# Kernel optimization log

Hardware: AMD Instinct MI355X
Metric: run time of the kernel (lower is better)

## Reference

```python
import jax, jax.numpy as jnp
import numpy as np

N = 50000       # nodes
E = 600000      # edges
F_IN = 500      # num_feature
H = 64          # hidden_dim (ODE state = 2*H)
C = 40          # num_class
T = 1.0         # integration time
STEPS = 4       # RK4 steps (16 ODE function evals)


def setup_inputs() -> dict:
    key = jax.random.key(0)
    ks = jax.random.split(key, 7)
    x = jax.random.normal(ks[0], (N, F_IN), dtype=jnp.float32)
    edge_src = jax.random.randint(ks[1], (E,), 0, N, dtype=jnp.int32)
    edge_dst = jax.random.randint(ks[2], (E,), 0, N, dtype=jnp.int32)
    edge_w = jax.random.uniform(ks[3], (E,), dtype=jnp.float32)
    m1_w = jax.random.normal(ks[4], (F_IN, H), dtype=jnp.float32) / np.sqrt(F_IN).astype(np.float32)
    m1_b = jnp.zeros((H,), jnp.float32)
    alpha_train = jnp.ones((N,), jnp.float32)  # alpha * ones(N) with alpha=1.0
    m2_w = jax.random.normal(ks[5], (H, C), dtype=jnp.float32) / np.sqrt(H).astype(np.float32)
    m2_b = jnp.zeros((C,), jnp.float32)
    return dict(x=x, edge_w=edge_w, m1_w=m1_w, m1_b=m1_b,
                alpha_train=alpha_train, m2_w=m2_w, m2_b=m2_b,
                edge_src=edge_src, edge_dst=edge_dst)


def spmm(edge_src, edge_dst, edge_w, z):
    # A @ z where A[i,j] = sum of edge_w over edges (src=i, dst=j)
    msg = edge_w[:, None] * z[edge_dst]           # [E, 2H]
    return jax.ops.segment_sum(msg, edge_src, num_segments=N)


def reference(x, edge_w, m1_w, m1_b, alpha_train, m2_w, m2_b, edge_src, edge_dst):
    # Encoder (dropout is identity in eval mode)
    h = x @ m1_w + m1_b                           # [N, H]
    h = jnp.concatenate([h, jnp.zeros_like(h)], axis=1)  # [N, 2H]
    x0 = jax.lax.stop_gradient(h)                 # x0 = x.clone().detach()
    alph = jax.nn.sigmoid(alpha_train)[:, None]   # [N, 1]

    def f(z):  # ODE RHS: sigmoid(alpha)*0.5*(A z - z) + x0
        az = spmm(edge_src, edge_dst, edge_w, z)
        return alph * 0.5 * (az - z) + x0

    dt = jnp.float32(T / STEPS)

    def step(z, _):
        k1 = f(z)
        k2 = f(z + 0.5 * dt * k1)
        k3 = f(z + 0.5 * dt * k2)
        k4 = f(z + dt * k3)
        return z + (dt / 6.0) * (k1 + 2.0 * k2 + 2.0 * k3 + k4), None

    z, _ = jax.lax.scan(step, h, None, length=STEPS)
    z = jax.nn.relu(z[:, :H])                     # first half of state
    return z @ m2_w + m2_b                        # [N, C]
```

## Files before the change

### kernel.cpp

```cpp
#include <hip/hip_runtime.h>
#include <hip/hip_fp16.h>

#define N_NODES 50000
#define N_EDGES 600000
#define F_IN    500
#define H_DIM   64
#define C_OUT   40
#define STEPS   4
#define NB_SCAN ((N_NODES + 255) / 256)
#define KTILES  16
#define DBINS   64

using half8 = __attribute__((ext_vector_type(8))) _Float16;
using f32x4 = __attribute__((ext_vector_type(4))) float;

__global__ __launch_bounds__(256) void bfrag_kernel(
    const float* __restrict__ W, __half* __restrict__ bfrag)
{
    int t = blockIdx.x * 256 + threadIdx.x;
    if (t >= KTILES * 4 * 64) return;
    int lane = t & 63;
    int c    = (t >> 6) & 3;
    int kt   = t >> 8;
    int col  = c * 16 + (lane & 15);
    int kb   = kt * 32 + (lane >> 4) * 8;
    union { uint4 u; __half h[8]; } v;
    #pragma unroll
    for (int j = 0; j < 8; ++j) {
        int k = kb + j;
        v.h[j] = (k < F_IN) ? __float2half(W[(size_t)k * H_DIM + col]) : __half(0.f);
    }
    *reinterpret_cast<uint4*>(bfrag + (size_t)t * 8) = v.u;
}

__global__ __launch_bounds__(256) void encoder_kernel(
    const float* __restrict__ x, const __half* __restrict__ bfrag,
    const float* __restrict__ b, __half* __restrict__ x0H,
    float* __restrict__ zF, __half* __restrict__ zH)
{
    __shared__ f32x4 red[2][64][4];

    int wave = threadIdx.x >> 6;
    int lane = threadIdx.x & 63;
    int pair = wave >> 1;
    int half = wave & 1;
    int rowl = lane & 15;
    int kg   = lane >> 4;
    int r0   = blockIdx.x * 32 + pair * 16;

    int gr = r0 + rowl; if (gr >= N_NODES) gr = N_NODES - 1;
    const float* xrow = x + (size_t)gr * F_IN;
    const uint4* bf = reinterpret_cast<const uint4*>(bfrag);

    int ktb = half * 8;

    float4 xv[16];
    #pragma unroll
    for (int ki = 0; ki < 8; ++ki) {
        int k0 = (ktb + ki) * 32 + kg * 8;
        xv[2 * ki]     = make_float4(0.f, 0.f, 0.f, 0.f);
        xv[2 * ki + 1] = make_float4(0.f, 0.f, 0.f, 0.f);
        if (k0 + 4 <= F_IN) xv[2 * ki]     = *reinterpret_cast<const float4*>(xrow + k0);
        if (k0 + 8 <= F_IN) xv[2 * ki + 1] = *reinterpret_cast<const float4*>(xrow + k0 + 4);
    }

    f32x4 acc[4];
    #pragma unroll
    for (int c = 0; c < 4; ++c) acc[c] = (f32x4){0.f, 0.f, 0.f, 0.f};

    #pragma unroll
    for (int ki = 0; ki < 8; ++ki) {
        int kt = ktb + ki;
        float4 xa = xv[2 * ki], xb = xv[2 * ki + 1];
        half8 a;
        a[0] = (_Float16)xa.x; a[1] = (_Float16)xa.y;
        a[2] = (_Float16)xa.z; a[3] = (_Float16)xa.w;
        a[4] = (_Float16)xb.x; a[5] = (_Float16)xb.y;
        a[6] = (_Float16)xb.z; a[7] = (_Float16)xb.w;
        #pragma unroll
        for (int c = 0; c < 4; ++c) {
            union { uint4 u; half8 h; } bv;
            bv.u = bf[(size_t)(kt * 4 + c) * 64 + lane];
            acc[c] = __builtin_amdgcn_mfma_f32_16x16x32_f16(a, bv.h, acc[c], 0, 0, 0);
        }
    }

    if (half == 1) {
        #pragma unroll
        for (int c = 0; c < 4; ++c) red[pair][lane][c] = acc[c];
    }
    __syncthreads();
    if (half == 0) {
        #pragma unroll
        for (int c = 0; c < 4; ++c) {
            f32x4 r = red[pair][lane][c];
            acc[c][0] += r[0]; acc[c][1] += r[1];
            acc[c][2] += r[2]; acc[c][3] += r[3];
        }
        #pragma unroll
        for (int c = 0; c < 4; ++c) {
            int col = c * 16 + rowl;
            float bias = b[col];
            #pragma unroll
            for (int r = 0; r < 4; ++r) {
                int grow = r0 + kg * 4 + r;
                if (grow < N_NODES) {
                    float v = acc[c][r] + bias;
                    size_t idx = (size_t)grow * H_DIM + col;
                    zF[idx]  = v;
                    __half hv = __float2half(v);
                    zH[idx]  = hv;
                    x0H[idx] = hv;
                }
            }
        }
    }
}

__global__ void hist_kernel(const int* __restrict__ src, int* __restrict__ counts)
{
    int e = blockIdx.x * 256 + threadIdx.x;
    if (e < N_EDGES) atomicAdd(&counts[src[e]], 1);
}

__global__ __launch_bounds__(256) void scanA_kernel(
    const int* __restrict__ counts, int* __restrict__ blockSums)
{
    __shared__ int red[256];
    int i = blockIdx.x * 256 + threadIdx.x;
    red[threadIdx.x] = (i < N_NODES) ? counts[i] : 0;
    __syncthreads();
    #pragma unroll
    for (int s = 128; s > 0; s >>= 1) {
        if (threadIdx.x < s) red[threadIdx.x] += red[threadIdx.x + s];
        __syncthreads();
    }
    if (threadIdx.x == 0) blockSums[blockIdx.x] = red[0];
}

__global__ __launch_bounds__(256) void scanB_kernel(
    const int* __restrict__ blockSums, int* __restrict__ blockBases)
{
    __shared__ int s[256];
    int tid = threadIdx.x;
    int v = (tid < NB_SCAN) ? blockSums[tid] : 0;
    s[tid] = v;
    __syncthreads();
    #pragma unroll
    for (int d = 1; d < 256; d <<= 1) {
        int t = (tid >= d) ? s[tid - d] : 0;
        __syncthreads();
        s[tid] += t;
        __syncthreads();
    }
    if (tid < NB_SCAN) blockBases[tid] = s[tid] - v;
}

__global__ __launch_bounds__(256) void scanC_kernel(
    const int* __restrict__ counts, const int* __restrict__ blockBases,
    int* __restrict__ off, int* __restrict__ cursor)
{
    __shared__ int s[256];
    int tid = threadIdx.x;
    int i = blockIdx.x * 256 + tid;
    int v = (i < N_NODES) ? counts[i] : 0;
    s[tid] = v;
    __syncthreads();
    #pragma unroll
    for (int d = 1; d < 256; d <<= 1) {
        int t = (tid >= d) ? s[tid - d] : 0;
        __syncthreads();
        s[tid] += t;
        __syncthreads();
    }
    if (i < N_NODES) {
        int excl = blockBases[blockIdx.x] + s[tid] - v;
        off[i] = excl;
        cursor[i] = excl;
        if (i == N_NODES - 1) off[N_NODES] = excl + v;
    }
}

__global__ void scatter_kernel(const int* __restrict__ src, const int* __restrict__ dst,
                               const float* __restrict__ w,
                               int* __restrict__ cursor, int2* __restrict__ epack)
{
    int e = blockIdx.x * 256 + threadIdx.x;
    if (e < N_EDGES) {
        int s = src[e];
        int p = atomicAdd(&cursor[s], 1);
        epack[p] = make_int2(dst[e] << 7, __float_as_int(w[e]));
    }
}

__global__ __launch_bounds__(256) void blockHist_kernel(
    const int* __restrict__ counts, int* __restrict__ blockBinCnt)
{
    __shared__ int lh[DBINS];
    int t = threadIdx.x;
    if (t < DBINS) lh[t] = 0;
    __syncthreads();
    int i = blockIdx.x * 256 + t;
    if (i < N_NODES) {
        int d = counts[i]; if (d > DBINS - 1) d = DBINS - 1;
        atomicAdd(&lh[d], 1);
    }
    __syncthreads();
    if (t < DBINS) blockBinCnt[blockIdx.x * DBINS + t] = lh[t];
}

__global__ __launch_bounds__(64) void degBase_kernel(
    const int* __restrict__ blockBinCnt, int* __restrict__ baseMat)
{
    __shared__ int tot[DBINS];
    __shared__ int start[DBINS];
    int d = threadIdx.x;
    int s = 0;
    for (int b = 0; b < NB_SCAN; ++b) s += blockBinCnt[b * DBINS + d];
    tot[d] = s;
    __syncthreads();
    if (d == 0) {
        int r = 0;
        for (int q = 0; q < DBINS; ++q) { start[q] = r; r += tot[q]; }
    }
    __syncthreads();
    int r = start[d];
    for (int b = 0; b < NB_SCAN; ++b) {
        baseMat[b * DBINS + d] = r;
        r += blockBinCnt[b * DBINS + d];
    }
}

__global__ __launch_bounds__(256) void degScatter_kernel(
    const int* __restrict__ counts, const int* __restrict__ baseMat,
    int* __restrict__ node_order)
{
    __shared__ int lcur[DBINS];
    int t = threadIdx.x;
    if (t < DBINS) lcur[t] = baseMat[blockIdx.x * DBINS + t];
    __syncthreads();
    int i = blockIdx.x * 256 + t;
    if (i < N_NODES) {
        int d = counts[i]; if (d > DBINS - 1) d = DBINS - 1;
        int p = atomicAdd(&lcur[d], 1);
        node_order[p] = i;
    }
}

template<int STAGE>
__global__ __launch_bounds__(256) void stage_kernel(
    const int* __restrict__ node_order,
    const int* __restrict__ off, const int2* __restrict__ epack,
    const __half* __restrict__ zsH, const __half* __restrict__ zH,
    const float* __restrict__ zbF, const __half* __restrict__ x0H,
    const float* __restrict__ alpha, __half* __restrict__ accH,
    __half* __restrict__ outH, float* __restrict__ outZ, float cnext)
{
    int nidx = blockIdx.x * 32 + (threadIdx.x >> 3);
    if (nidx >= N_NODES) return;
    int node = node_order[nidx];
    int cb = (threadIdx.x & 7) << 4;
    int c  = cb >> 1;

    int jb = off[node], je = off[node + 1];
    const char* rdB = reinterpret_cast<const char*>(zsH);

    union H4 { uint4 u; __half2 h[4]; };

    float azA[8], azB[8];
    #pragma unroll
    for (int i = 0; i < 8; ++i) { azA[i] = 0.f; azB[i] = 0.f; }

#define ACC8(dst, V, W)                                                    \
    {                                                                      \
        float2 f0 = __half22float2((V).h[0]);                              \
        float2 f1 = __half22float2((V).h[1]);                              \
        float2 f2 = __half22float2((V).h[2]);                              \
        float2 f3 = __half22float2((V).h[3]);                              \
        dst[0] = fmaf(W, f0.x, dst[0]); dst[1] = fmaf(W, f0.y, dst[1]);    \
        dst[2] = fmaf(W, f1.x, dst[2]); dst[3] = fmaf(W, f1.y, dst[3]);    \
        dst[4] = fmaf(W, f2.x, dst[4]); dst[5] = fmaf(W, f2.y, dst[5]);    \
        dst[6] = fmaf(W, f3.x, dst[6]); dst[7] = fmaf(W, f3.y, dst[7]);    \
    }

    int j = jb;
    for (; j + 3 < je; j += 4) {
        int2 e0 = epack[j];
        int2 e1 = epack[j + 1];
        int2 e2 = epack[j + 2];
        int2 e3 = epack[j + 3];
        H4 v0, v1, v2, v3;
        v0.u = *reinterpret_cast<const uint4*>(rdB + (size_t)(unsigned)e0.x + cb);
        v1.u = *reinterpret_cast<const uint4*>(rdB + (size_t)(unsigned)e1.x + cb);
        v2.u = *reinterpret_cast<const uint4*>(rdB + (size_t)(unsigned)e2.x + cb);
        v3.u = *reinterpret_cast<const uint4*>(rdB + (size_t)(unsigned)e3.x + cb);
        float w0 = __int_as_float(e0.y), w1 = __int_as_float(e1.y);
        float w2 = __int_as_float(e2.y), w3 = __int_as_float(e3.y);
        ACC8(azA, v0, w0);
        ACC8(azB, v1, w1);
        ACC8(azA, v2, w2);
        ACC8(azB, v3, w3);
    }
    for (; j < je; ++j) {
        int2 e0 = epack[j];
        H4 v0;
        v0.u = *reinterpret_cast<const uint4*>(rdB + (size_t)(unsigned)e0.x + cb);
        float w0 = __int_as_float(e0.y);
        ACC8(azA, v0, w0);
    }
#undef ACC8

    float az[8];
    #pragma unroll
    for (int i = 0; i < 8; ++i) az[i] = azA[i] + azB[i];

    size_t idx = (size_t)node * H_DIM + c;
    H4 sr; sr.u = *reinterpret_cast<const uint4*>(zsH + idx);
    float s[8];
    {
        float2 f0 = __half22float2(sr.h[0]), f1 = __half22float2(sr.h[1]);
        float2 f2 = __half22float2(sr.h[2]), f3 = __half22float2(sr.h[3]);
        s[0] = f0.x; s[1] = f0.y; s[2] = f1.x; s[3] = f1.y;
        s[4] = f2.x; s[5] = f2.y; s[6] = f3.x; s[7] = f3.y;
    }
    H4 xr; xr.u = *reinterpret_cast<const uint4*>(x0H + idx);
    float xv[8];
    {
        float2 f0 = __half22float2(xr.h[0]), f1 = __half22float2(xr.h[1]);
        float2 f2 = __half22float2(xr.h[2]), f3 = __half22float2(xr.h[3]);
        xv[0] = f0.x; xv[1] = f0.y; xv[2] = f1.x; xv[3] = f1.y;
        xv[4] = f2.x; xv[5] = f2.y; xv[6] = f3.x; xv[7] = f3.y;
    }
    float a = 0.5f / (1.f + __expf(-alpha[node]));

    float k[8];
    #pragma unroll
    for (int i = 0; i < 8; ++i) k[i] = fmaf(a, az[i] - s[i], xv[i]);

    float o[8];
    if constexpr (STAGE == 0) {
        H4 aw;
        aw.h[0] = __float22half2_rn(make_float2(k[0], k[1]));
        aw.h[1] = __float22half2_rn(make_float2(k[2], k[3]));
        aw.h[2] = __float22half2_rn(make_float2(k[4], k[5]));
        aw.h[3] = __float22half2_rn(make_float2(k[6], k[7]));
        *reinterpret_cast<uint4*>(accH + idx) = aw.u;
        #pragma unroll
        for (int i = 0; i < 8; ++i) o[i] = fmaf(cnext, k[i], s[i]);
    } else if constexpr (STAGE == 1 || STAGE == 2) {
        H4 ar; ar.u = *reinterpret_cast<const uint4*>(accH + idx);
        float av[8];
        {
            float2 f0 = __half22float2(ar.h[0]), f1 = __half22float2(ar.h[1]);
            float2 f2 = __half22float2(ar.h[2]), f3 = __half22float2(ar.h[3]);
            av[0] = f0.x; av[1] = f0.y; av[2] = f1.x; av[3] = f1.y;
            av[4] = f2.x; av[5] = f2.y; av[6] = f3.x; av[7] = f3.y;
        }
        #pragma unroll
        for (int i = 0; i < 8; ++i) av[i] = fmaf(2.f, k[i], av[i]);
        H4 aw;
        aw.h[0] = __float22half2_rn(make_float2(av[0], av[1]));
        aw.h[1] = __float22half2_rn(make_float2(av[2], av[3]));
        aw.h[2] = __float22half2_rn(make_float2(av[4], av[5]));
        aw.h[3] = __float22half2_rn(make_float2(av[6], av[7]));
        *reinterpret_cast<uint4*>(accH + idx) = aw.u;
        H4 br; br.u = *reinterpret_cast<const uint4*>(zH + idx);
        float bv[8];
        {
            float2 f0 = __half22float2(br.h[0]), f1 = __half22float2(br.h[1]);
            float2 f2 = __half22float2(br.h[2]), f3 = __half22float2(br.h[3]);
            bv[0] = f0.x; bv[1] = f0.y; bv[2] = f1.x; bv[3] = f1.y;
            bv[4] = f2.x; bv[5] = f2.y; bv[6] = f3.x; bv[7] = f3.y;
        }
        #pragma unroll
        for (int i = 0; i < 8; ++i) o[i] = fmaf(cnext, k[i], bv[i]);
    } else {
        H4 ar; ar.u = *reinterpret_cast<const uint4*>(accH + idx);
        float av[8];
        {
            float2 f0 = __half22float2(ar.h[0]), f1 = __half22float2(ar.h[1]);
            float2 f2 = __half22float2(ar.h[2]), f3 = __half22float2(ar.h[3]);
            av[0] = f0.x; av[1] = f0.y; av[2] = f1.x; av[3] = f1.y;
            av[4] = f2.x; av[5] = f2.y; av[6] = f3.x; av[7] = f3.y;
        }
        float4 zb0 = *reinterpret_cast<const float4*>(zbF + idx);
        float4 zb1 = *reinterpret_cast<const float4*>(zbF + idx + 4);
        float zb[8] = {zb0.x, zb0.y, zb0.z, zb0.w, zb1.x, zb1.y, zb1.z, zb1.w};
        #pragma unroll
        for (int i = 0; i < 8; ++i) o[i] = fmaf(cnext, av[i] + k[i], zb[i]);
        float4 oz0 = make_float4(o[0], o[1], o[2], o[3]);
        float4 oz1 = make_float4(o[4], o[5], o[6], o[7]);
        *reinterpret_cast<float4*>(outZ + idx)     = oz0;
        *reinterpret_cast<float4*>(outZ + idx + 4) = oz1;
    }
    H4 sv;
    sv.h[0] = __float22half2_rn(make_float2(o[0], o[1]));
    sv.h[1] = __float22half2_rn(make_float2(o[2], o[3]));
    sv.h[2] = __float22half2_rn(make_float2(o[4], o[5]));
    sv.h[3] = __float22half2_rn(make_float2(o[6], o[7]));
    *reinterpret_cast<uint4*>(outH + idx) = sv.u;
}

__global__ __launch_bounds__(256) void decoder_kernel(
    const float* __restrict__ z, const float* __restrict__ W2,
    const float* __restrict__ b2, float* __restrict__ out)
{
    __shared__ float zsm[4][H_DIM];
    int lane = threadIdx.x & 63;
    int w    = threadIdx.x >> 6;
    int node = blockIdx.x * 4 + w;
    int ld   = node >= N_NODES ? N_NODES - 1 : node;
    float zv = z[(size_t)ld * H_DIM + lane];
    zsm[w][lane] = zv > 0.f ? zv : 0.f;
    __syncthreads();
    if (node < N_NODES && lane < C_OUT) {
        float acc = b2[lane];
        #pragma unroll
        for (int k = 0; k < H_DIM; ++k)
            acc = fmaf(zsm[w][k], W2[k * C_OUT + lane], acc);
        out[(size_t)node * C_OUT + lane] = acc;
    }
}

extern "C" void kernel_launch(void* const* d_in, const int* in_sizes, int n_in,
                              void* d_out, int out_size, void* d_ws, size_t ws_size,
                              hipStream_t stream)
{
    const float* x     = (const float*)d_in[0];
    const float* ew    = (const float*)d_in[1];
    const float* m1w   = (const float*)d_in[2];
    const float* m1b   = (const float*)d_in[3];
    const float* alpha = (const float*)d_in[4];
    const float* m2w   = (const float*)d_in[5];
    const float* m2b   = (const float*)d_in[6];
    const int*   esrc  = (const int*)d_in[7];
    const int*   edst  = (const int*)d_in[8];
    float* out = (float*)d_out;

    char* ws = (char*)d_ws;
    size_t o = 0;
    auto alloc = [&](size_t bytes) -> void* {
        void* p = ws + o;
        o = (o + bytes + 255) & ~(size_t)255;
        return p;
    };
    float*  z      = (float*)alloc((size_t)N_NODES * H_DIM * 4);
    __half* x0H    = (__half*)alloc((size_t)N_NODES * H_DIM * 2);
    __half* zH     = (__half*)alloc((size_t)N_NODES * H_DIM * 2);
    __half* ztAH   = (__half*)alloc((size_t)N_NODES * H_DIM * 2);
    __half* ztBH   = (__half*)alloc((size_t)N_NODES * H_DIM * 2);
    __half* accH   = (__half*)alloc((size_t)N_NODES * H_DIM * 2);
    __half* bfrag  = (__half*)alloc((size_t)KTILES * 4 * 64 * 8 * 2);
    int*    counts = (int*)alloc((size_t)N_NODES * 4);
    int*    off    = (int*)alloc((size_t)(N_NODES + 1) * 4);
    int*    cursor = (int*)alloc((size_t)N_NODES * 4);
    int*    bsums  = (int*)alloc((size_t)NB_SCAN * 4);
    int*    bbases = (int*)alloc((size_t)NB_SCAN * 4);
    int*    bbc    = (int*)alloc((size_t)NB_SCAN * DBINS * 4);
    int*    bmat   = (int*)alloc((size_t)NB_SCAN * DBINS * 4);
    int*    nodeOrd= (int*)alloc((size_t)N_NODES * 4);
    int2*   epack  = (int2*)alloc((size_t)N_EDGES * 8);

    hipMemsetAsync(counts, 0, (size_t)N_NODES * 4, stream);
    hist_kernel<<<(N_EDGES + 255) / 256, 256, 0, stream>>>(esrc, counts);
    scanA_kernel<<<NB_SCAN, 256, 0, stream>>>(counts, bsums);
    scanB_kernel<<<1, 256, 0, stream>>>(bsums, bbases);
    scanC_kernel<<<NB_SCAN, 256, 0, stream>>>(counts, bbases, off, cursor);
    scatter_kernel<<<(N_EDGES + 255) / 256, 256, 0, stream>>>(esrc, edst, ew, cursor, epack);

    blockHist_kernel<<<NB_SCAN, 256, 0, stream>>>(counts, bbc);
    degBase_kernel<<<1, 64, 0, stream>>>(bbc, bmat);
    degScatter_kernel<<<NB_SCAN, 256, 0, stream>>>(counts, bmat, nodeOrd);

    bfrag_kernel<<<(KTILES * 4 * 64 + 255) / 256, 256, 0, stream>>>(m1w, bfrag);
    encoder_kernel<<<(N_NODES + 31) / 32, 256, 0, stream>>>(x, bfrag, m1b, x0H, z, zH);

    const float dt = 1.0f / STEPS;
    int sgrid = (N_NODES + 31) / 32;
    for (int step = 0; step < STEPS; ++step) {
        stage_kernel<0><<<sgrid, 256, 0, stream>>>(nodeOrd, off, epack, zH,   zH, nullptr, x0H, alpha, accH, ztAH, nullptr, 0.5f * dt);
        stage_kernel<1><<<sgrid, 256, 0, stream>>>(nodeOrd, off, epack, ztAH, zH, nullptr, x0H, alpha, accH, ztBH, nullptr, 0.5f * dt);
        stage_kernel<2><<<sgrid, 256, 0, stream>>>(nodeOrd, off, epack, ztBH, zH, nullptr, x0H, alpha, accH, ztAH, nullptr, dt);
        stage_kernel<3><<<sgrid, 256, 0, stream>>>(nodeOrd, off, epack, ztAH, zH, z,       x0H, alpha, accH, zH,   z,       dt / 6.0f);
    }

    decoder_kernel<<<(N_NODES + 3) / 4, 256, 0, stream>>>(z, m2w, m2b, out);
}
```

Baseline: 440.0 us.

## Store node state in degree-sorted order to make stage accesses contiguous

Renumbers nodes by the degree-sorted order. The encoder writes state rows at permuted positions, edge destinations are remapped through an inverse permutation, and the decoder un-permutes when writing output. Per-node metadata (edge range and sigmoid alpha coefficient) is precomputed into permuted arrays. Stage kernels then read their own rows and metadata contiguously, with no indirection through node_order and no per-call exp. This adds a few cheap setup kernels and scattered writes in the encoder, and gathered neighbor reads stay random.

New measurement: 424.0 us. -3.6%, faster.

```diff
diff --git a/kernel.cpp b/kernel.cpp
--- a/kernel.cpp
+++ b/kernel.cpp
@@ -35,8 +35,8 @@
 
 __global__ __launch_bounds__(256) void encoder_kernel(
     const float* __restrict__ x, const __half* __restrict__ bfrag,
-    const float* __restrict__ b, __half* __restrict__ x0H,
-    float* __restrict__ zF, __half* __restrict__ zH)
+    const float* __restrict__ b, const int* __restrict__ invOrd,
+    __half* __restrict__ x0H, float* __restrict__ zF, __half* __restrict__ zH)
 {
     __shared__ f32x4 red[2][64][4];
 
@@ -98,15 +98,15 @@
             acc[c][2] += r[2]; acc[c][3] += r[3];
         }
         #pragma unroll
-        for (int c = 0; c < 4; ++c) {
-            int col = c * 16 + rowl;
-            float bias = b[col];
-            #pragma unroll
-            for (int r = 0; r < 4; ++r) {
-                int grow = r0 + kg * 4 + r;
-                if (grow < N_NODES) {
-                    float v = acc[c][r] + bias;
-                    size_t idx = (size_t)grow * H_DIM + col;
+        for (int r = 0; r < 4; ++r) {
+            int grow = r0 + kg * 4 + r;
+            if (grow < N_NODES) {
+                int prow = invOrd[grow];
+                #pragma unroll
+                for (int c = 0; c < 4; ++c) {
+                    int col = c * 16 + rowl;
+                    float v = acc[c][r] + b[col];
+                    size_t idx = (size_t)prow * H_DIM + col;
                     zF[idx]  = v;
                     __half hv = __float2half(v);
                     zH[idx]  = hv;
@@ -181,18 +181,6 @@
     }
 }
 
-__global__ void scatter_kernel(const int* __restrict__ src, const int* __restrict__ dst,
-                               const float* __restrict__ w,
-                               int* __restrict__ cursor, int2* __restrict__ epack)
-{
-    int e = blockIdx.x * 256 + threadIdx.x;
-    if (e < N_EDGES) {
-        int s = src[e];
-        int p = atomicAdd(&cursor[s], 1);
-        epack[p] = make_int2(dst[e] << 7, __float_as_int(w[e]));
-    }
-}
-
 __global__ __launch_bounds__(256) void blockHist_kernel(
     const int* __restrict__ counts, int* __restrict__ blockBinCnt)
 {
@@ -247,22 +235,54 @@
     }
 }
 
+__global__ void invOrd_kernel(const int* __restrict__ nodeOrd, int* __restrict__ invOrd)
+{
+    int i = blockIdx.x * 256 + threadIdx.x;
+    if (i < N_NODES) invOrd[nodeOrd[i]] = i;
+}
+
+__global__ void permMeta_kernel(const int* __restrict__ nodeOrd,
+                                const int* __restrict__ off,
+                                const float* __restrict__ alpha,
+                                int* __restrict__ jbArr, int* __restrict__ jeArr,
+                                float* __restrict__ acoArr)
+{
+    int i = blockIdx.x * 256 + threadIdx.x;
+    if (i < N_NODES) {
+        int old = nodeOrd[i];
+        jbArr[i]  = off[old];
+        jeArr[i]  = off[old + 1];
+        acoArr[i] = 0.5f / (1.f + __expf(-alpha[old]));
+    }
+}
+
+__global__ void scatter_kernel(const int* __restrict__ src, const int* __restrict__ dst,
+                               const float* __restrict__ w, const int* __restrict__ invOrd,
+                               int* __restrict__ cursor, int2* __restrict__ epack)
+{
+    int e = blockIdx.x * 256 + threadIdx.x;
+    if (e < N_EDGES) {
+        int s = src[e];
+        int p = atomicAdd(&cursor[s], 1);
+        epack[p] = make_int2(invOrd[dst[e]] << 7, __float_as_int(w[e]));
+    }
+}
+
 template<int STAGE>
 __global__ __launch_bounds__(256) void stage_kernel(
-    const int* __restrict__ node_order,
-    const int* __restrict__ off, const int2* __restrict__ epack,
+    const int* __restrict__ jbArr, const int* __restrict__ jeArr,
+    const float* __restrict__ acoArr, const int2* __restrict__ epack,
     const __half* __restrict__ zsH, const __half* __restrict__ zH,
     const float* __restrict__ zbF, const __half* __restrict__ x0H,
-    const float* __restrict__ alpha, __half* __restrict__ accH,
+    __half* __restrict__ accH,
     __half* __restrict__ outH, float* __restrict__ outZ, float cnext)
 {
     int nidx = blockIdx.x * 32 + (threadIdx.x >> 3);
     if (nidx >= N_NODES) return;
-    int node = node_order[nidx];
     int cb = (threadIdx.x & 7) << 4;
     int c  = cb >> 1;
 
-    int jb = off[node], je = off[node + 1];
+    int jb = jbArr[nidx], je = jeArr[nidx];
     const char* rdB = reinterpret_cast<const char*>(zsH);
 
     union H4 { uint4 u; __half2 h[4]; };
@@ -314,7 +334,7 @@
     #pragma unroll
     for (int i = 0; i < 8; ++i) az[i] = azA[i] + azB[i];
 
-    size_t idx = (size_t)node * H_DIM + c;
+    size_t idx = (size_t)nidx * H_DIM + c;
     H4 sr; sr.u = *reinterpret_cast<const uint4*>(zsH + idx);
     float s[8];
     {
@@ -331,7 +351,7 @@
         xv[0] = f0.x; xv[1] = f0.y; xv[2] = f1.x; xv[3] = f1.y;
         xv[4] = f2.x; xv[5] = f2.y; xv[6] = f3.x; xv[7] = f3.y;
     }
-    float a = 0.5f / (1.f + __expf(-alpha[node]));
+    float a = acoArr[nidx];
 
     float k[8];
     #pragma unroll
@@ -402,8 +422,9 @@
 }
 
 __global__ __launch_bounds__(256) void decoder_kernel(
-    const float* __restrict__ z, const float* __restrict__ W2,
-    const float* __restrict__ b2, float* __restrict__ out)
+    const float* __restrict__ z, const int* __restrict__ nodeOrd,
+    const float* __restrict__ W2, const float* __restrict__ b2,
+    float* __restrict__ out)
 {
     __shared__ float zsm[4][H_DIM];
     int lane = threadIdx.x & 63;
@@ -418,7 +439,7 @@
         #pragma unroll
         for (int k = 0; k < H_DIM; ++k)
             acc = fmaf(zsm[w][k], W2[k * C_OUT + lane], acc);
-        out[(size_t)node * C_OUT + lane] = acc;
+        out[(size_t)nodeOrd[node] * C_OUT + lane] = acc;
     }
 }
 
@@ -459,6 +480,10 @@
     int*    bbc    = (int*)alloc((size_t)NB_SCAN * DBINS * 4);
     int*    bmat   = (int*)alloc((size_t)NB_SCAN * DBINS * 4);
     int*    nodeOrd= (int*)alloc((size_t)N_NODES * 4);
+    int*    invOrd = (int*)alloc((size_t)N_NODES * 4);
+    int*    jbArr  = (int*)alloc((size_t)N_NODES * 4);
+    int*    jeArr  = (int*)alloc((size_t)N_NODES * 4);
+    float*  acoArr = (float*)alloc((size_t)N_NODES * 4);
     int2*   epack  = (int2*)alloc((size_t)N_EDGES * 8);
 
     hipMemsetAsync(counts, 0, (size_t)N_NODES * 4, stream);
@@ -466,23 +491,26 @@
     scanA_kernel<<<NB_SCAN, 256, 0, stream>>>(counts, bsums);
     scanB_kernel<<<1, 256, 0, stream>>>(bsums, bbases);
     scanC_kernel<<<NB_SCAN, 256, 0, stream>>>(counts, bbases, off, cursor);
-    scatter_kernel<<<(N_EDGES + 255) / 256, 256, 0, stream>>>(esrc, edst, ew, cursor, epack);
 
     blockHist_kernel<<<NB_SCAN, 256, 0, stream>>>(counts, bbc);
     degBase_kernel<<<1, 64, 0, stream>>>(bbc, bmat);
     degScatter_kernel<<<NB_SCAN, 256, 0, stream>>>(counts, bmat, nodeOrd);
+    invOrd_kernel<<<NB_SCAN, 256, 0, stream>>>(nodeOrd, invOrd);
+    permMeta_kernel<<<NB_SCAN, 256, 0, stream>>>(nodeOrd, off, alpha, jbArr, jeArr, acoArr);
+
+    scatter_kernel<<<(N_EDGES + 255) / 256, 256, 0, stream>>>(esrc, edst, ew, invOrd, cursor, epack);
 
     bfrag_kernel<<<(KTILES * 4 * 64 + 255) / 256, 256, 0, stream>>>(m1w, bfrag);
-    encoder_kernel<<<(N_NODES + 31) / 32, 256, 0, stream>>>(x, bfrag, m1b, x0H, z, zH);
+    encoder_kernel<<<(N_NODES + 31) / 32, 256, 0, stream>>>(x, bfrag, m1b, invOrd, x0H, z, zH);
 
     const float dt = 1.0f / STEPS;
     int sgrid = (N_NODES + 31) / 32;
     for (int step = 0; step < STEPS; ++step) {
-        stage_kernel<0><<<sgrid, 256, 0, stream>>>(nodeOrd, off, epack, zH,   zH, nullptr, x0H, alpha, accH, ztAH, nullptr, 0.5f * dt);
-        stage_kernel<1><<<sgrid, 256, 0, stream>>>(nodeOrd, off, epack, ztAH, zH, nullptr, x0H, alpha, accH, ztBH, nullptr, 0.5f * dt);
-        stage_kernel<2><<<sgrid, 256, 0, stream>>>(nodeOrd, off, epack, ztBH, zH, nullptr, x0H, alpha, accH, ztAH, nullptr, dt);
-        stage_kernel<3><<<sgrid, 256, 0, stream>>>(nodeOrd, off, epack, ztAH, zH, z,       x0H, alpha, accH, zH,   z,       dt / 6.0f);
-    }
-
-    decoder_kernel<<<(N_NODES + 3) / 4, 256, 0, stream>>>(z, m2w, m2b, out);
-}
+        stage_kernel<0><<<sgrid, 256, 0, stream>>>(jbArr, jeArr, acoArr, epack, zH,   zH, nullptr, x0H, accH, ztAH, nullptr, 0.5f * dt);
+        stage_kernel<1><<<sgrid, 256, 0, stream>>>(jbArr, jeArr, acoArr, epack, ztAH, zH, nullptr, x0H, accH, ztBH, nullptr, 0.5f * dt);
+        stage_kernel<2><<<sgrid, 256, 0, stream>>>(jbArr, jeArr, acoArr, epack, ztBH, zH, nullptr, x0H, accH, ztAH, nullptr, dt);
+        stage_kernel<3><<<sgrid, 256, 0, stream>>>(jbArr, jeArr, acoArr, epack, ztAH, zH, z,       x0H, accH, zH,   z,       dt / 6.0f);
+    }
+
+    decoder_kernel<<<(N_NODES + 3) / 4, 256, 0, stream>>>(z, nodeOrd, m2w, m2b, out);
+}
```
